# Kernel optimization log

Measured on AMD Instinct MI355X. Metric: run time of the kernel, lower is better.

## Reference

```python
import jax, jax.numpy as jnp
import numpy as np

B = 4096
D_FULL, D_T1, D_T2 = 1024, 512, 512
N_SPEC, N_SHARED = 4, 4
HID, OUT = 512, 256


def _expert_params(key, n_experts, d_in):
    k1, k2, k3, k4 = jax.random.split(key, 4)
    s1 = 1.0 / np.sqrt(d_in)
    s2 = 1.0 / np.sqrt(HID)
    return {
        'W1': jax.random.uniform(k1, (n_experts, d_in, HID), jnp.float32, -s1, s1),
        'b1': jax.random.uniform(k2, (n_experts, HID), jnp.float32, -s1, s1),
        'W2': jax.random.uniform(k3, (n_experts, HID, OUT), jnp.float32, -s2, s2),
        'b2': jax.random.uniform(k4, (n_experts, OUT), jnp.float32, -s2, s2),
    }


def setup_inputs() -> dict:
    key = jax.random.key(0)
    ks = jax.random.split(key, 12)
    x_full = jax.random.normal(ks[0], (B, D_FULL), jnp.float32)
    x_task1 = jax.random.normal(ks[1], (B, D_T1), jnp.float32)
    x_task2 = jax.random.normal(ks[2], (B, D_T2), jnp.float32)
    ps = _expert_params(ks[3], N_SHARED, D_FULL)
    p1 = _expert_params(ks[4], N_SPEC, D_T1)
    p2 = _expert_params(ks[5], N_SPEC, D_T2)
    sg = 1.0 / np.sqrt(D_FULL)
    s1 = 1.0 / np.sqrt(D_T1)
    s2 = 1.0 / np.sqrt(D_T2)
    return {
        'x_full': x_full, 'x_task1': x_task1, 'x_task2': x_task2,
        'sh_W1': ps['W1'], 'sh_b1': ps['b1'], 'sh_W2': ps['W2'], 'sh_b2': ps['b2'],
        't1_W1': p1['W1'], 't1_b1': p1['b1'], 't1_W2': p1['W2'], 't1_b2': p1['b2'],
        't2_W1': p2['W1'], 't2_b1': p2['b1'], 't2_W2': p2['W2'], 't2_b2': p2['b2'],
        'gsh_W': jax.random.uniform(ks[6], (D_FULL, 2 * N_SPEC + N_SHARED), jnp.float32, -sg, sg),
        'gsh_b': jax.random.uniform(ks[7], (2 * N_SPEC + N_SHARED,), jnp.float32, -sg, sg),
        'g1_W': jax.random.uniform(ks[8], (D_T1, N_SPEC + N_SHARED), jnp.float32, -s1, s1),
        'g1_b': jax.random.uniform(ks[9], (N_SPEC + N_SHARED,), jnp.float32, -s1, s1),
        'g2_W': jax.random.uniform(ks[10], (D_T2, N_SPEC + N_SHARED), jnp.float32, -s2, s2),
        'g2_b': jax.random.uniform(ks[11], (N_SPEC + N_SHARED,), jnp.float32, -s2, s2),
    }


def _experts(x, W1, b1, W2, b2):
    # x: [B, D]; W1: [E, D, H] -> out [E, B, OUT]
    h = jax.nn.relu(jnp.einsum('bd,edh->ebh', x, W1) + b1[:, None, :])
    return jax.nn.relu(jnp.einsum('ebh,eho->ebo', h, W2) + b2[:, None, :])


def reference(x_full, x_task1, x_task2,
              sh_W1, sh_b1, sh_W2, sh_b2,
              t1_W1, t1_b1, t1_W2, t1_b2,
              t2_W1, t2_b1, t2_W2, t2_b2,
              gsh_W, gsh_b, g1_W, g1_b, g2_W, g2_b):
    eo_shared = _experts(x_full, sh_W1, sh_b1, sh_W2, sh_b2)    # [Es, B, OUT]
    eo_t1 = _experts(x_task1, t1_W1, t1_b1, t1_W2, t1_b2)       # [Et, B, OUT]
    eo_t2 = _experts(x_task2, t2_W1, t2_b1, t2_W2, t2_b2)       # [Et, B, OUT]

    g1 = jax.nn.softmax(x_task1 @ g1_W + g1_b, axis=1)          # [B, Et+Es]
    out1 = jnp.einsum('ebc,be->bc', jnp.concatenate([eo_t1, eo_shared], axis=0), g1)

    g2 = jax.nn.softmax(x_task2 @ g2_W + g2_b, axis=1)
    out2 = jnp.einsum('ebc,be->bc', jnp.concatenate([eo_t2, eo_shared], axis=0), g2)

    gsh = jax.nn.softmax(x_full @ gsh_W + gsh_b, axis=1)        # [B, 2Et+Es]
    out_sh = jnp.einsum('ebc,be->bc', jnp.concatenate([eo_t1, eo_t2, eo_shared], axis=0), gsh)

    return (out_sh, out1, out2)
```

## Files before the change

### kernel.cpp

```cpp
#include <hip/hip_runtime.h>

typedef unsigned short u16;
typedef __attribute__((ext_vector_type(8))) short short8;
typedef __attribute__((ext_vector_type(4))) float f32x4;

#define GL2LDS16(src, dst) __builtin_amdgcn_global_load_lds( \
    (const __attribute__((address_space(1))) void*)(src),    \
    (__attribute__((address_space(3))) void*)(dst), 16, 0, 0)

__device__ __forceinline__ u16 f2bf(float f) {
  union { float f; unsigned u; } v; v.f = f;
  unsigned r = v.u + 0x7fffu + ((v.u >> 16) & 1u);
  return (u16)(r >> 16);
}
__device__ __forceinline__ float bf2f(u16 h) {
  union { unsigned u; float f; } v; v.u = ((unsigned)h) << 16; return v.f;
}

__global__ void k_gates_cvt(const float* __restrict__ xf, const float* __restrict__ x1,
                            const float* __restrict__ x2,
                            const float* __restrict__ gshW, const float* __restrict__ gshB,
                            const float* __restrict__ g1W, const float* __restrict__ g1B,
                            const float* __restrict__ g2W, const float* __restrict__ g2B,
                            u16* __restrict__ xfb, u16* __restrict__ x1b, u16* __restrict__ x2b,
                            float* __restrict__ gsh, float* __restrict__ g1o,
                            float* __restrict__ g2o) {
  const int b = blockIdx.x, lane = threadIdx.x;
  float s[12];
#pragma unroll
  for (int j = 0; j < 12; ++j) s[j] = 0.f;
  {
    const float* xr = xf + (size_t)b * 1024;
    u16* xw = xfb + (size_t)b * 1024;
    for (int k = lane; k < 1024; k += 64) {
      float v = xr[k];
      xw[k] = f2bf(v);
      const float* wr = gshW + (size_t)k * 12;
#pragma unroll
      for (int j = 0; j < 12; ++j) s[j] += v * wr[j];
    }
  }
  float u[8], w[8];
#pragma unroll
  for (int j = 0; j < 8; ++j) { u[j] = 0.f; w[j] = 0.f; }
  {
    const float* xr1 = x1 + (size_t)b * 512;
    const float* xr2 = x2 + (size_t)b * 512;
    u16* xw1 = x1b + (size_t)b * 512;
    u16* xw2 = x2b + (size_t)b * 512;
    for (int k = lane; k < 512; k += 64) {
      float v1 = xr1[k], v2 = xr2[k];
      xw1[k] = f2bf(v1); xw2[k] = f2bf(v2);
      const float* w1r = g1W + (size_t)k * 8;
      const float* w2r = g2W + (size_t)k * 8;
#pragma unroll
      for (int j = 0; j < 8; ++j) { u[j] += v1 * w1r[j]; w[j] += v2 * w2r[j]; }
    }
  }
#pragma unroll
  for (int off = 32; off >= 1; off >>= 1) {
#pragma unroll
    for (int j = 0; j < 12; ++j) s[j] += __shfl_xor(s[j], off, 64);
#pragma unroll
    for (int j = 0; j < 8; ++j) { u[j] += __shfl_xor(u[j], off, 64); w[j] += __shfl_xor(w[j], off, 64); }
  }
  if (lane == 0) {
    float m = -1e30f, tot = 0.f;
#pragma unroll
    for (int j = 0; j < 12; ++j) { s[j] += gshB[j]; m = fmaxf(m, s[j]); }
#pragma unroll
    for (int j = 0; j < 12; ++j) { s[j] = __expf(s[j] - m); tot += s[j]; }
    float inv = 1.f / tot;
#pragma unroll
    for (int j = 0; j < 12; ++j) gsh[(size_t)b * 12 + j] = s[j] * inv;
    m = -1e30f; tot = 0.f;
#pragma unroll
    for (int j = 0; j < 8; ++j) { u[j] += g1B[j]; m = fmaxf(m, u[j]); }
#pragma unroll
    for (int j = 0; j < 8; ++j) { u[j] = __expf(u[j] - m); tot += u[j]; }
    inv = 1.f / tot;
#pragma unroll
    for (int j = 0; j < 8; ++j) g1o[(size_t)b * 8 + j] = u[j] * inv;
    m = -1e30f; tot = 0.f;
#pragma unroll
    for (int j = 0; j < 8; ++j) { w[j] += g2B[j]; m = fmaxf(m, w[j]); }
#pragma unroll
    for (int j = 0; j < 8; ++j) { w[j] = __expf(w[j] - m); tot += w[j]; }
    inv = 1.f / tot;
#pragma unroll
    for (int j = 0; j < 8; ++j) g2o[(size_t)b * 8 + j] = w[j] * inv;
  }
}

struct TD { const float* src; u16* dst; int lgTps; int lgNtx; int R; int C; int tileBase; };
struct TArgs { TD d[6]; };

__global__ void k_transpose_all(TArgs ta) {
  __shared__ float tile[32][33];
  const int x = blockIdx.x;
  int di = 0;
#pragma unroll
  for (int i = 1; i < 6; ++i)
    if (x >= ta.d[i].tileBase) di = i;
  TD d = ta.d[di];
  const int local = x - d.tileBase;
  const int slice = local >> d.lgTps;
  const int ti = local & ((1 << d.lgTps) - 1);
  const int tx = ti & ((1 << d.lgNtx) - 1);
  const int ty = ti >> d.lgNtx;
  const float* src = d.src + (size_t)slice * d.R * d.C;
  u16* dst = d.dst + (size_t)slice * d.R * d.C;
  const int c0 = tx * 32, r0 = ty * 32;
  const int ttx = threadIdx.x, tty = threadIdx.y;
#pragma unroll
  for (int i = tty; i < 32; i += 8)
    tile[i][ttx] = src[(size_t)(r0 + i) * d.C + (c0 + ttx)];
  __syncthreads();
#pragma unroll
  for (int i = tty; i < 32; i += 8)
    dst[(size_t)(c0 + i) * d.R + (r0 + ttx)] = f2bf(tile[ttx][i]);
}

struct GemmDesc {
  const u16* A;
  const u16* BT;
  const float* bias;
  u16* C;
  int K;
  int N;
};
struct GemmArgs { GemmDesc d[12]; };

__global__ __launch_bounds__(512) void k_gemm8(GemmArgs args) {
  __shared__ __align__(16) u16 As[3 * 16384];
  __shared__ __align__(16) u16 Bs[3 * 8192];

  GemmDesc g = args.d[blockIdx.y];
  const int K = g.K, N = g.N;
  const int ntN = N >> 7;
  const int lg = (ntN == 4) ? 2 : 1;
  const int bx = blockIdx.x;
  const int row0 = (bx >> lg) << 8;
  const int col0 = (bx & (ntN - 1)) << 7;

  const int tid = threadIdx.x;
  const int lane = tid & 63;
  const int wid = tid >> 6;
  const int wm = wid >> 1;
  const int wn = wid & 1;
  const int lrow = lane & 15;
  const int lkq = lane >> 4;
  const int sw = lrow & 7;
  const int cx0 = lkq ^ sw;
  const int cx1 = (4 | lkq) ^ sw;

  int aoffs[4], boffs[4];
#pragma unroll
  for (int m = 0; m < 4; ++m) aoffs[m] = ((wm << 6) + (m << 4) + lrow) << 3;
#pragma unroll
  for (int n = 0; n < 4; ++n) boffs[n] = ((wn << 6) + (n << 4) + lrow) << 3;

  auto stageA = [&](int s, int kt, int j) {
    const int cb = (j << 9) + (wid << 6);
    const int c = cb + lane;
    const int r = c >> 3;
    const int gch = (c & 7) ^ (r & 7);
    GL2LDS16(g.A + (size_t)(row0 + r) * K + (kt << 6) + (gch << 3),
             &As[s * 16384 + cb * 8]);
  };
  auto stageB = [&](int s, int kt, int j) {
    const int cb = (j << 9) + (wid << 6);
    const int c = cb + lane;
    const int r = c >> 3;
    const int gch = (c & 7) ^ (r & 7);
    GL2LDS16(g.BT + (size_t)(col0 + r) * K + (kt << 6) + (gch << 3),
             &Bs[s * 8192 + cb * 8]);
  };

  f32x4 acc[4][4];
#pragma unroll
  for (int m = 0; m < 4; ++m)
#pragma unroll
    for (int n = 0; n < 4; ++n)
      acc[m][n] = (f32x4){0.f, 0.f, 0.f, 0.f};

  const int T = K >> 6;
#pragma unroll
  for (int j = 0; j < 4; ++j) stageA(0, 0, j);
#pragma unroll
  for (int j = 0; j < 2; ++j) stageB(0, 0, j);
#pragma unroll
  for (int j = 0; j < 4; ++j) stageA(1, 1, j);
#pragma unroll
  for (int j = 0; j < 2; ++j) stageB(1, 1, j);
  asm volatile("s_waitcnt vmcnt(6)" ::: "memory");
  __builtin_amdgcn_s_barrier();

  int slot = 0;
  for (int t = 0; t < T; ++t) {
    const u16* Asl = &As[slot * 16384];
    const u16* Bsl = &Bs[slot * 8192];
    const int s2 = (slot >= 1) ? slot - 1 : 2;
    short8 a[4], b[4];

#pragma unroll
    for (int m = 0; m < 4; ++m) a[m] = *(const short8*)&Asl[(aoffs[m] | cx0) << 3];
#pragma unroll
    for (int n = 0; n < 4; ++n) b[n] = *(const short8*)&Bsl[(boffs[n] | cx0) << 3];
    if (t + 2 < T) { stageA(s2, t + 2, 0); stageA(s2, t + 2, 1); stageB(s2, t + 2, 0); }
    __builtin_amdgcn_s_barrier();
    asm volatile("s_waitcnt lgkmcnt(0)" ::: "memory");
    __builtin_amdgcn_sched_barrier(0);
    __builtin_amdgcn_s_setprio(1);
#pragma unroll
    for (int m = 0; m < 4; ++m)
#pragma unroll
      for (int n = 0; n < 4; ++n)
        acc[m][n] = __builtin_amdgcn_mfma_f32_16x16x32_bf16(a[m], b[n], acc[m][n], 0, 0, 0);
    __builtin_amdgcn_s_setprio(0);
    __builtin_amdgcn_s_barrier();

#pragma unroll
    for (int m = 0; m < 4; ++m) a[m] = *(const short8*)&Asl[(aoffs[m] | cx1) << 3];
#pragma unroll
    for (int n = 0; n < 4; ++n) b[n] = *(const short8*)&Bsl[(boffs[n] | cx1) << 3];
    if (t + 2 < T) { stageA(s2, t + 2, 2); stageA(s2, t + 2, 3); stageB(s2, t + 2, 1); }
    __builtin_amdgcn_s_barrier();
    asm volatile("s_waitcnt lgkmcnt(0)" ::: "memory");
    __builtin_amdgcn_sched_barrier(0);
    __builtin_amdgcn_s_setprio(1);
#pragma unroll
    for (int m = 0; m < 4; ++m)
#pragma unroll
      for (int n = 0; n < 4; ++n)
        acc[m][n] = __builtin_amdgcn_mfma_f32_16x16x32_bf16(a[m], b[n], acc[m][n], 0, 0, 0);
    __builtin_amdgcn_s_setprio(0);
    asm volatile("s_waitcnt vmcnt(6)" ::: "memory");
    __builtin_amdgcn_s_barrier();

    slot = (slot == 2) ? 0 : slot + 1;
  }

  const int rb = lkq << 2;
#pragma unroll
  for (int n = 0; n < 4; ++n) {
    const int gc = col0 + (wn << 6) + (n << 4) + lrow;
    const float bv = g.bias[gc];
#pragma unroll
    for (int m = 0; m < 4; ++m) {
      const int gr = row0 + (wm << 6) + (m << 4) + rb;
#pragma unroll
      for (int j = 0; j < 4; ++j) {
        float o = fmaxf(acc[m][n][j] + bv, 0.f);
        g.C[(size_t)(gr + j) * N + gc] = f2bf(o);
      }
    }
  }
}

__global__ void k_reduce(const u16* __restrict__ OutB, const float* __restrict__ gsh,
                         const float* __restrict__ g1, const float* __restrict__ g2,
                         float* __restrict__ out) {
  int t = blockIdx.x * 256 + threadIdx.x;
  int b = t >> 5;
  int c0 = (t & 31) << 3;
  float wsh[12], w1[8], w2[8];
#pragma unroll
  for (int j = 0; j < 12; ++j) wsh[j] = gsh[(size_t)b * 12 + j];
#pragma unroll
  for (int j = 0; j < 8; ++j) { w1[j] = g1[(size_t)b * 8 + j]; w2[j] = g2[(size_t)b * 8 + j]; }
  float ash[8] = {0, 0, 0, 0, 0, 0, 0, 0};
  float a1[8] = {0, 0, 0, 0, 0, 0, 0, 0};
  float a2[8] = {0, 0, 0, 0, 0, 0, 0, 0};
#pragma unroll
  for (int e = 0; e < 12; ++e) {
    short8 v = *(const short8*)&OutB[((size_t)e * 4096 + b) * 256 + c0];
    float f[8];
#pragma unroll
    for (int i = 0; i < 8; ++i) f[i] = bf2f((u16)v[i]);
#pragma unroll
    for (int i = 0; i < 8; ++i) ash[i] += wsh[e] * f[i];
    if (e < 4) {
#pragma unroll
      for (int i = 0; i < 8; ++i) a1[i] += w1[e] * f[i];
    } else if (e < 8) {
#pragma unroll
      for (int i = 0; i < 8; ++i) a2[i] += w2[e - 4] * f[i];
    } else {
#pragma unroll
      for (int i = 0; i < 8; ++i) a1[i] += w1[e - 4] * f[i];
#pragma unroll
      for (int i = 0; i < 8; ++i) a2[i] += w2[e - 4] * f[i];
    }
  }
  size_t base = (size_t)b * 256 + c0;
  float4* o;
  o = (float4*)(out + base);
  o[0] = make_float4(ash[0], ash[1], ash[2], ash[3]);
  o[1] = make_float4(ash[4], ash[5], ash[6], ash[7]);
  o = (float4*)(out + 4096ull * 256 + base);
  o[0] = make_float4(a1[0], a1[1], a1[2], a1[3]);
  o[1] = make_float4(a1[4], a1[5], a1[6], a1[7]);
  o = (float4*)(out + 2ull * 4096 * 256 + base);
  o[0] = make_float4(a2[0], a2[1], a2[2], a2[3]);
  o[1] = make_float4(a2[4], a2[5], a2[6], a2[7]);
}

extern "C" void kernel_launch(void* const* d_in, const int* in_sizes, int n_in,
                              void* d_out, int out_size, void* d_ws, size_t ws_size,
                              hipStream_t stream) {
  const float* x_full = (const float*)d_in[0];
  const float* x_t1 = (const float*)d_in[1];
  const float* x_t2 = (const float*)d_in[2];
  const float* sh_W1 = (const float*)d_in[3];
  const float* sh_b1 = (const float*)d_in[4];
  const float* sh_W2 = (const float*)d_in[5];
  const float* sh_b2 = (const float*)d_in[6];
  const float* t1_W1 = (const float*)d_in[7];
  const float* t1_b1 = (const float*)d_in[8];
  const float* t1_W2 = (const float*)d_in[9];
  const float* t1_b2 = (const float*)d_in[10];
  const float* t2_W1 = (const float*)d_in[11];
  const float* t2_b1 = (const float*)d_in[12];
  const float* t2_W2 = (const float*)d_in[13];
  const float* t2_b2 = (const float*)d_in[14];
  const float* gsh_W = (const float*)d_in[15];
  const float* gsh_b = (const float*)d_in[16];
  const float* g1_W = (const float*)d_in[17];
  const float* g1_b = (const float*)d_in[18];
  const float* g2_W = (const float*)d_in[19];
  const float* g2_b = (const float*)d_in[20];

  char* ws = (char*)d_ws;
  size_t off = 0;
  auto alloc = [&](size_t bytes) -> void* {
    void* p = ws + off;
    off += (bytes + 255) & ~(size_t)255;
    return p;
  };
  u16* xf_b = (u16*)alloc(4096ull * 1024 * 2);
  u16* x1_b = (u16*)alloc(4096ull * 512 * 2);
  u16* x2_b = (u16*)alloc(4096ull * 512 * 2);
  u16* w1t_t1 = (u16*)alloc(4ull * 512 * 512 * 2);
  u16* w1t_t2 = (u16*)alloc(4ull * 512 * 512 * 2);
  u16* w1t_sh = (u16*)alloc(4ull * 512 * 1024 * 2);
  u16* w2t = (u16*)alloc(12ull * 256 * 512 * 2);
  u16* H = (u16*)alloc(12ull * 4096 * 512 * 2);
  u16* OutB = (u16*)alloc(12ull * 4096 * 256 * 2);
  float* gshv = (float*)alloc(4096ull * 12 * 4);
  float* g1v = (float*)alloc(4096ull * 8 * 4);
  float* g2v = (float*)alloc(4096ull * 8 * 4);

  k_gates_cvt<<<4096, 64, 0, stream>>>(x_full, x_t1, x_t2, gsh_W, gsh_b, g1_W, g1_b, g2_W, g2_b,
                                       xf_b, x1_b, x2_b, gshv, g1v, g2v);

  TArgs ta;
  ta.d[0] = TD{t1_W1, w1t_t1, 8, 4, 512, 512, 0};
  ta.d[1] = TD{t2_W1, w1t_t2, 8, 4, 512, 512, 1024};
  ta.d[2] = TD{sh_W1, w1t_sh, 9, 4, 1024, 512, 2048};
  ta.d[3] = TD{t1_W2, w2t, 7, 3, 512, 256, 4096};
  ta.d[4] = TD{t2_W2, w2t + 4ull * 256 * 512, 7, 3, 512, 256, 4608};
  ta.d[5] = TD{sh_W2, w2t + 8ull * 256 * 512, 7, 3, 512, 256, 5120};
  k_transpose_all<<<5632, dim3(32, 8), 0, stream>>>(ta);

  GemmArgs ga1;
  for (int e = 0; e < 4; ++e) {
    ga1.d[e] = GemmDesc{xf_b, w1t_sh + (size_t)e * 512 * 1024, sh_b1 + e * 512,
                        H + (size_t)(8 + e) * 4096 * 512, 1024, 512};
    ga1.d[4 + e] = GemmDesc{x1_b, w1t_t1 + (size_t)e * 512 * 512, t1_b1 + e * 512,
                            H + (size_t)e * 4096 * 512, 512, 512};
    ga1.d[8 + e] = GemmDesc{x2_b, w1t_t2 + (size_t)e * 512 * 512, t2_b1 + e * 512,
                            H + (size_t)(4 + e) * 4096 * 512, 512, 512};
  }
  k_gemm8<<<dim3(64, 12), 512, 0, stream>>>(ga1);

  GemmArgs ga2;
  for (int e = 0; e < 12; ++e) {
    const float* bias = (e < 4) ? (t1_b2 + e * 256)
                      : (e < 8) ? (t2_b2 + (e - 4) * 256)
                                : (sh_b2 + (e - 8) * 256);
    ga2.d[e] = GemmDesc{H + (size_t)e * 4096 * 512, w2t + (size_t)e * 256 * 512, bias,
                        OutB + (size_t)e * 4096 * 256, 512, 256};
  }
  k_gemm8<<<dim3(32, 12), 512, 0, stream>>>(ga2);

  k_reduce<<<512, 256, 0, stream>>>(OutB, gshv, g1v, g2v, (float*)d_out);
}
```

Baseline: 117.9 us.

## Replace 256x128 GEMM tile with 256x256 tile and double-buffered half-stage pipeline

The batched expert GEMM kernel now uses 256x256 output tiles per 512-thread block (8x4 MFMA accumulators per wave) instead of 256x128. The LDS staging becomes two buffers, with A and B loaded in halves interleaved across eight phases per two K-steps, and uses new swizzle patterns. The larger tile raises arithmetic intensity and halves the number of blocks. In exchange, register pressure is higher, only one block fits per CU, and grids shrink to 384 and 192 blocks, which may underfill the 256 CUs.

```diff
diff --git a/kernel.cpp b/kernel.cpp
--- a/kernel.cpp
+++ b/kernel.cpp
@@ -128,130 +128,131 @@
   u16* C;
   int K;
   int N;
+  int iters;
 };
 struct GemmArgs { GemmDesc d[12]; };
 
-__global__ __launch_bounds__(512) void k_gemm8(GemmArgs args) {
-  __shared__ __align__(16) u16 As[3 * 16384];
-  __shared__ __align__(16) u16 Bs[3 * 8192];
+#define PHASE(BUF, KS, MH, ...)                                                   \
+  {                                                                               \
+    const char* AsB = (const char*)As + (BUF) * 32768;                            \
+    const char* BsB = (const char*)Bs + (BUF) * 32768 + (KS) * 16384;             \
+    if ((MH) == 0) {                                                              \
+      _Pragma("unroll") for (int ni = 0; ni < 4; ++ni)                            \
+          b[ni] = *(const short8*)(BsB + boff[ni]);                               \
+    }                                                                             \
+    _Pragma("unroll") for (int q = 0; q < 4; ++q)                                 \
+        a[q] = *(const short8*)(AsB + (aoff[(MH) * 4 + q] ^ ((KS) * 64)));        \
+    __VA_ARGS__;                                                                  \
+    __builtin_amdgcn_s_barrier();                                                 \
+    asm volatile("s_waitcnt lgkmcnt(0)" ::: "memory");                            \
+    __builtin_amdgcn_sched_barrier(0);                                            \
+    __builtin_amdgcn_s_setprio(1);                                                \
+    _Pragma("unroll") for (int q = 0; q < 4; ++q)                                 \
+        _Pragma("unroll") for (int ni = 0; ni < 4; ++ni)                          \
+            acc[(MH) * 4 + q][ni] = __builtin_amdgcn_mfma_f32_16x16x32_bf16(      \
+                a[q], b[ni], acc[(MH) * 4 + q][ni], 0, 0, 0);                     \
+    __builtin_amdgcn_s_setprio(0);                                                \
+  }
+
+__global__ __launch_bounds__(512, 1) void k_gemm256(GemmArgs args) {
+  __shared__ __align__(16) u16 As[32768];
+  __shared__ __align__(16) u16 Bs[32768];
 
   GemmDesc g = args.d[blockIdx.y];
-  const int K = g.K, N = g.N;
-  const int ntN = N >> 7;
-  const int lg = (ntN == 4) ? 2 : 1;
+  const int K = g.K, N = g.N, iters = g.iters;
+  const int ntN = N >> 8;
+  const int lg = (ntN == 2) ? 1 : 0;
   const int bx = blockIdx.x;
   const int row0 = (bx >> lg) << 8;
-  const int col0 = (bx & (ntN - 1)) << 7;
+  const int col0 = (bx & (ntN - 1)) << 8;
 
   const int tid = threadIdx.x;
   const int lane = tid & 63;
   const int wid = tid >> 6;
-  const int wm = wid >> 1;
-  const int wn = wid & 1;
+  const int wm = wid & 1;
+  const int wn = wid >> 1;
   const int lrow = lane & 15;
   const int lkq = lane >> 4;
-  const int sw = lrow & 7;
-  const int cx0 = lkq ^ sw;
-  const int cx1 = (4 | lkq) ^ sw;
-
-  int aoffs[4], boffs[4];
-#pragma unroll
-  for (int m = 0; m < 4; ++m) aoffs[m] = ((wm << 6) + (m << 4) + lrow) << 3;
-#pragma unroll
-  for (int n = 0; n < 4; ++n) boffs[n] = ((wn << 6) + (n << 4) + lrow) << 3;
-
-  auto stageA = [&](int s, int kt, int j) {
-    const int cb = (j << 9) + (wid << 6);
-    const int c = cb + lane;
-    const int r = c >> 3;
-    const int gch = (c & 7) ^ (r & 7);
-    GL2LDS16(g.A + (size_t)(row0 + r) * K + (kt << 6) + (gch << 3),
-             &As[s * 16384 + cb * 8]);
+
+  int aoff[8], boff[4];
+#pragma unroll
+  for (int mi = 0; mi < 8; ++mi)
+    aoff[mi] = wm * 16384 + (mi * 16 + lrow) * 128 + ((lkq ^ (lrow & 7)) * 16);
+#pragma unroll
+  for (int ni = 0; ni < 4; ++ni)
+    boff[ni] = (wn * 64 + ni * 16 + lrow) * 64 + ((lkq ^ ((lrow >> 1) & 3)) * 16);
+
+  auto stageAhalf = [&](int buf, int half, int kt) {
+#pragma unroll
+    for (int j = 0; j < 2; ++j) {
+      const int cb = (wid * 2 + j) * 64;
+      const int c = cb + lane;
+      const int r = c >> 3;
+      const int cir = (c & 7) ^ (r & 7);
+      GL2LDS16(g.A + (size_t)(row0 + half * 128 + r) * K + kt * 64 + cir * 8,
+               &As[(buf * 2048 + half * 1024 + cb) * 8]);
+    }
   };
-  auto stageB = [&](int s, int kt, int j) {
-    const int cb = (j << 9) + (wid << 6);
-    const int c = cb + lane;
-    const int r = c >> 3;
-    const int gch = (c & 7) ^ (r & 7);
-    GL2LDS16(g.BT + (size_t)(col0 + r) * K + (kt << 6) + (gch << 3),
-             &Bs[s * 8192 + cb * 8]);
+  auto stageBhalf = [&](int buf, int ks, int kt) {
+#pragma unroll
+    for (int j = 0; j < 2; ++j) {
+      const int cb = (wid * 2 + j) * 64;
+      const int c = cb + lane;
+      const int r = c >> 2;
+      const int cir = (c & 3) ^ ((r >> 1) & 3);
+      GL2LDS16(g.BT + (size_t)(col0 + r) * K + kt * 64 + ks * 32 + cir * 8,
+               &Bs[(buf * 2048 + ks * 1024 + cb) * 8]);
+    }
   };
 
-  f32x4 acc[4][4];
-#pragma unroll
-  for (int m = 0; m < 4; ++m)
+  f32x4 acc[8][4];
+#pragma unroll
+  for (int m = 0; m < 8; ++m)
 #pragma unroll
     for (int n = 0; n < 4; ++n)
       acc[m][n] = (f32x4){0.f, 0.f, 0.f, 0.f};
 
-  const int T = K >> 6;
-#pragma unroll
-  for (int j = 0; j < 4; ++j) stageA(0, 0, j);
-#pragma unroll
-  for (int j = 0; j < 2; ++j) stageB(0, 0, j);
-#pragma unroll
-  for (int j = 0; j < 4; ++j) stageA(1, 1, j);
-#pragma unroll
-  for (int j = 0; j < 2; ++j) stageB(1, 1, j);
-  asm volatile("s_waitcnt vmcnt(6)" ::: "memory");
+  stageBhalf(0, 0, 0); stageBhalf(0, 1, 0);
+  stageAhalf(0, 0, 0); stageAhalf(0, 1, 0);
+  stageBhalf(1, 0, 1); stageBhalf(1, 1, 1);
+  asm volatile("s_waitcnt vmcnt(4)" ::: "memory");
   __builtin_amdgcn_s_barrier();
 
-  int slot = 0;
-  for (int t = 0; t < T; ++t) {
-    const u16* Asl = &As[slot * 16384];
-    const u16* Bsl = &Bs[slot * 8192];
-    const int s2 = (slot >= 1) ? slot - 1 : 2;
-    short8 a[4], b[4];
-
-#pragma unroll
-    for (int m = 0; m < 4; ++m) a[m] = *(const short8*)&Asl[(aoffs[m] | cx0) << 3];
-#pragma unroll
-    for (int n = 0; n < 4; ++n) b[n] = *(const short8*)&Bsl[(boffs[n] | cx0) << 3];
-    if (t + 2 < T) { stageA(s2, t + 2, 0); stageA(s2, t + 2, 1); stageB(s2, t + 2, 0); }
-    __builtin_amdgcn_s_barrier();
-    asm volatile("s_waitcnt lgkmcnt(0)" ::: "memory");
-    __builtin_amdgcn_sched_barrier(0);
-    __builtin_amdgcn_s_setprio(1);
-#pragma unroll
-    for (int m = 0; m < 4; ++m)
-#pragma unroll
-      for (int n = 0; n < 4; ++n)
-        acc[m][n] = __builtin_amdgcn_mfma_f32_16x16x32_bf16(a[m], b[n], acc[m][n], 0, 0, 0);
-    __builtin_amdgcn_s_setprio(0);
-    __builtin_amdgcn_s_barrier();
-
-#pragma unroll
-    for (int m = 0; m < 4; ++m) a[m] = *(const short8*)&Asl[(aoffs[m] | cx1) << 3];
-#pragma unroll
-    for (int n = 0; n < 4; ++n) b[n] = *(const short8*)&Bsl[(boffs[n] | cx1) << 3];
-    if (t + 2 < T) { stageA(s2, t + 2, 2); stageA(s2, t + 2, 3); stageB(s2, t + 2, 1); }
-    __builtin_amdgcn_s_barrier();
-    asm volatile("s_waitcnt lgkmcnt(0)" ::: "memory");
-    __builtin_amdgcn_sched_barrier(0);
-    __builtin_amdgcn_s_setprio(1);
-#pragma unroll
-    for (int m = 0; m < 4; ++m)
-#pragma unroll
-      for (int n = 0; n < 4; ++n)
-        acc[m][n] = __builtin_amdgcn_mfma_f32_16x16x32_bf16(a[m], b[n], acc[m][n], 0, 0, 0);
-    __builtin_amdgcn_s_setprio(0);
-    asm volatile("s_waitcnt vmcnt(6)" ::: "memory");
-    __builtin_amdgcn_s_barrier();
-
-    slot = (slot == 2) ? 0 : slot + 1;
-  }
-
-  const int rb = lkq << 2;
-#pragma unroll
-  for (int n = 0; n < 4; ++n) {
-    const int gc = col0 + (wn << 6) + (n << 4) + lrow;
+  short8 a[4], b[4];
+  for (int i = 0; i < iters; ++i) {
+    const int t1 = 2 * i + 1;
+    const bool nl = (i + 1 < iters);
+    PHASE(0, 0, 0, stageAhalf(1, 0, t1));
+    __builtin_amdgcn_s_barrier();
+    PHASE(0, 0, 1, stageAhalf(1, 1, t1));
+    __builtin_amdgcn_s_barrier();
+    PHASE(0, 1, 0, if (nl) stageBhalf(0, 0, t1 + 1));
+    __builtin_amdgcn_s_barrier();
+    PHASE(0, 1, 1, if (nl) stageBhalf(0, 1, t1 + 1));
+    if (nl) { asm volatile("s_waitcnt vmcnt(4)" ::: "memory"); }
+    else    { asm volatile("s_waitcnt vmcnt(0)" ::: "memory"); }
+    __builtin_amdgcn_s_barrier();
+    PHASE(1, 0, 0, if (nl) stageAhalf(0, 0, t1 + 1));
+    __builtin_amdgcn_s_barrier();
+    PHASE(1, 0, 1, if (nl) stageAhalf(0, 1, t1 + 1));
+    __builtin_amdgcn_s_barrier();
+    PHASE(1, 1, 0, if (nl) stageBhalf(1, 0, t1 + 2));
+    __builtin_amdgcn_s_barrier();
+    PHASE(1, 1, 1, if (nl) stageBhalf(1, 1, t1 + 2));
+    asm volatile("s_waitcnt vmcnt(4)" ::: "memory");
+    __builtin_amdgcn_s_barrier();
+  }
+
+#pragma unroll
+  for (int ni = 0; ni < 4; ++ni) {
+    const int gc = col0 + wn * 64 + ni * 16 + lrow;
     const float bv = g.bias[gc];
 #pragma unroll
-    for (int m = 0; m < 4; ++m) {
-      const int gr = row0 + (wm << 6) + (m << 4) + rb;
+    for (int mi = 0; mi < 8; ++mi) {
+      const int gr = row0 + wm * 128 + mi * 16 + lkq * 4;
 #pragma unroll
       for (int j = 0; j < 4; ++j) {
-        float o = fmaxf(acc[m][n][j] + bv, 0.f);
+        float o = fmaxf(acc[mi][ni][j] + bv, 0.f);
         g.C[(size_t)(gr + j) * N + gc] = f2bf(o);
       }
     }
@@ -366,13 +367,13 @@
   GemmArgs ga1;
   for (int e = 0; e < 4; ++e) {
     ga1.d[e] = GemmDesc{xf_b, w1t_sh + (size_t)e * 512 * 1024, sh_b1 + e * 512,
-                        H + (size_t)(8 + e) * 4096 * 512, 1024, 512};
+                        H + (size_t)(8 + e) * 4096 * 512, 1024, 512, 8};
     ga1.d[4 + e] = GemmDesc{x1_b, w1t_t1 + (size_t)e * 512 * 512, t1_b1 + e * 512,
-                            H + (size_t)e * 4096 * 512, 512, 512};
+                            H + (size_t)e * 4096 * 512, 512, 512, 4};
     ga1.d[8 + e] = GemmDesc{x2_b, w1t_t2 + (size_t)e * 512 * 512, t2_b1 + e * 512,
-                            H + (size_t)(4 + e) * 4096 * 512, 512, 512};
-  }
-  k_gemm8<<<dim3(64, 12), 512, 0, stream>>>(ga1);
+                            H + (size_t)(4 + e) * 4096 * 512, 512, 512, 4};
+  }
+  k_gemm256<<<dim3(32, 12), 512, 0, stream>>>(ga1);
 
   GemmArgs ga2;
   for (int e = 0; e < 12; ++e) {
@@ -380,9 +381,9 @@
                       : (e < 8) ? (t2_b2 + (e - 4) * 256)
                                 : (sh_b2 + (e - 8) * 256);
     ga2.d[e] = GemmDesc{H + (size_t)e * 4096 * 512, w2t + (size_t)e * 256 * 512, bias,
-                        OutB + (size_t)e * 4096 * 256, 512, 256};
-  }
-  k_gemm8<<<dim3(32, 12), 512, 0, stream>>>(ga2);
+                        OutB + (size_t)e * 4096 * 256, 512, 256, 4};
+  }
+  k_gemm256<<<dim3(16, 12), 512, 0, stream>>>(ga2);
 
   k_reduce<<<512, 256, 0, stream>>>(OutB, gshv, g1v, g2v, (float*)d_out);
 }
```

Result: faster. 113.2 us (-4.0%).

## Replace 256x128 triple-buffered GEMM with 128x256 double-buffered BK=32 kernel

Applied to the files above, without the earlier changes.

The GEMM kernel moves from a 256x128 output tile with K-step 64 and a three-slot LDS pipeline to a 128x256 tile with K-step 32 and two buffers. LDS drops to 48KB per block, and launch_bounds(512,4) asks for higher occupancy. Each iteration now ends with a full vmcnt(0) wait and a barrier, and the loop trip count T is passed in from the host. The aim is more resident blocks to hide latency, at the cost of more barriers per unit of K and a shallower prefetch.

```diff
diff --git a/kernel.cpp b/kernel.cpp
--- a/kernel.cpp
+++ b/kernel.cpp
@@ -128,53 +128,60 @@
   u16* C;
   int K;
   int N;
+  int T;
 };
 struct GemmArgs { GemmDesc d[12]; };
 
-__global__ __launch_bounds__(512) void k_gemm8(GemmArgs args) {
-  __shared__ __align__(16) u16 As[3 * 16384];
-  __shared__ __align__(16) u16 Bs[3 * 8192];
+#define BARR __builtin_amdgcn_s_barrier()
+#define WAITL0                                                   \
+  {                                                              \
+    asm volatile("s_waitcnt lgkmcnt(0)" ::: "memory");           \
+    __builtin_amdgcn_sched_barrier(0);                           \
+  }
+#define WAITV0 asm volatile("s_waitcnt vmcnt(0)" ::: "memory")
+
+__global__ __launch_bounds__(512, 4) void k_gemm128(GemmArgs args) {
+  __shared__ __align__(16) u16 As[2 * 128 * 32];
+  __shared__ __align__(16) u16 Bs[2 * 256 * 32];
 
   GemmDesc g = args.d[blockIdx.y];
-  const int K = g.K, N = g.N;
-  const int ntN = N >> 7;
-  const int lg = (ntN == 4) ? 2 : 1;
+  const int K = g.K, N = g.N, T = g.T;
+  const int ntN = N >> 8;
   const int bx = blockIdx.x;
-  const int row0 = (bx >> lg) << 8;
-  const int col0 = (bx & (ntN - 1)) << 7;
+  const int nt = bx & (ntN - 1);
+  const int bt = (ntN == 2) ? (bx >> 1) : bx;
+  const int row0 = bt << 7;
+  const int col0 = nt << 8;
 
   const int tid = threadIdx.x;
   const int lane = tid & 63;
   const int wid = tid >> 6;
-  const int wm = wid >> 1;
-  const int wn = wid & 1;
+  const int wm = wid & 1;
+  const int wn = wid >> 1;
   const int lrow = lane & 15;
   const int lkq = lane >> 4;
-  const int sw = lrow & 7;
-  const int cx0 = lkq ^ sw;
-  const int cx1 = (4 | lkq) ^ sw;
-
-  int aoffs[4], boffs[4];
-#pragma unroll
-  for (int m = 0; m < 4; ++m) aoffs[m] = ((wm << 6) + (m << 4) + lrow) << 3;
-#pragma unroll
-  for (int n = 0; n < 4; ++n) boffs[n] = ((wn << 6) + (n << 4) + lrow) << 3;
-
-  auto stageA = [&](int s, int kt, int j) {
-    const int cb = (j << 9) + (wid << 6);
-    const int c = cb + lane;
-    const int r = c >> 3;
-    const int gch = (c & 7) ^ (r & 7);
-    GL2LDS16(g.A + (size_t)(row0 + r) * K + (kt << 6) + (gch << 3),
-             &As[s * 16384 + cb * 8]);
-  };
-  auto stageB = [&](int s, int kt, int j) {
-    const int cb = (j << 9) + (wid << 6);
-    const int c = cb + lane;
-    const int r = c >> 3;
-    const int gch = (c & 7) ^ (r & 7);
-    GL2LDS16(g.BT + (size_t)(col0 + r) * K + (kt << 6) + (gch << 3),
-             &Bs[s * 8192 + cb * 8]);
+
+  const int csw = (lkq ^ (lrow & 3)) * 16;
+  int aoff[4], boff[4];
+#pragma unroll
+  for (int mi = 0; mi < 4; ++mi) aoff[mi] = (wm * 64 + mi * 16 + lrow) * 64 + csw;
+#pragma unroll
+  for (int ni = 0; ni < 4; ++ni) boff[ni] = (wn * 64 + ni * 16 + lrow) * 64 + csw;
+
+  const int ar = tid >> 2;
+  const int acs = (tid & 3) ^ (ar & 3);
+  const u16* aSrc = g.A + (size_t)(row0 + ar) * K + acs * 8;
+  const int br0 = tid >> 2;
+  const int bc0 = (tid & 3) ^ (br0 & 3);
+  const u16* bSrc0 = g.BT + (size_t)(col0 + br0) * K + bc0 * 8;
+  const int br1 = 128 + (tid >> 2);
+  const int bc1 = (tid & 3) ^ (br1 & 3);
+  const u16* bSrc1 = g.BT + (size_t)(col0 + br1) * K + bc1 * 8;
+
+  auto STAGE = [&](int buf, int t) {
+    GL2LDS16(aSrc + (size_t)t * 32, &As[buf * 4096 + tid * 8]);
+    GL2LDS16(bSrc0 + (size_t)t * 32, &Bs[buf * 8192 + tid * 8]);
+    GL2LDS16(bSrc1 + (size_t)t * 32, &Bs[buf * 8192 + 4096 + tid * 8]);
   };
 
   f32x4 acc[4][4];
@@ -184,74 +191,52 @@
     for (int n = 0; n < 4; ++n)
       acc[m][n] = (f32x4){0.f, 0.f, 0.f, 0.f};
 
-  const int T = K >> 6;
-#pragma unroll
-  for (int j = 0; j < 4; ++j) stageA(0, 0, j);
-#pragma unroll
-  for (int j = 0; j < 2; ++j) stageB(0, 0, j);
-#pragma unroll
-  for (int j = 0; j < 4; ++j) stageA(1, 1, j);
-#pragma unroll
-  for (int j = 0; j < 2; ++j) stageB(1, 1, j);
-  asm volatile("s_waitcnt vmcnt(6)" ::: "memory");
-  __builtin_amdgcn_s_barrier();
-
-  int slot = 0;
+  STAGE(0, 0);
+  WAITV0;
+  BARR;
+
   for (int t = 0; t < T; ++t) {
-    const u16* Asl = &As[slot * 16384];
-    const u16* Bsl = &Bs[slot * 8192];
-    const int s2 = (slot >= 1) ? slot - 1 : 2;
-    short8 a[4], b[4];
-
-#pragma unroll
-    for (int m = 0; m < 4; ++m) a[m] = *(const short8*)&Asl[(aoffs[m] | cx0) << 3];
-#pragma unroll
-    for (int n = 0; n < 4; ++n) b[n] = *(const short8*)&Bsl[(boffs[n] | cx0) << 3];
-    if (t + 2 < T) { stageA(s2, t + 2, 0); stageA(s2, t + 2, 1); stageB(s2, t + 2, 0); }
-    __builtin_amdgcn_s_barrier();
-    asm volatile("s_waitcnt lgkmcnt(0)" ::: "memory");
-    __builtin_amdgcn_sched_barrier(0);
+    const int buf = t & 1;
+    const char* Ab = (const char*)As + buf * 8192;
+    const char* Bb = (const char*)Bs + buf * 16384;
+    short8 a0, a1, b[4];
+#pragma unroll
+    for (int ni = 0; ni < 4; ++ni) b[ni] = *(const short8*)(Bb + boff[ni]);
+    a0 = *(const short8*)(Ab + aoff[0]);
+    a1 = *(const short8*)(Ab + aoff[1]);
+    if (t + 1 < T) STAGE(buf ^ 1, t + 1);
+    WAITL0;
     __builtin_amdgcn_s_setprio(1);
 #pragma unroll
-    for (int m = 0; m < 4; ++m)
-#pragma unroll
-      for (int n = 0; n < 4; ++n)
-        acc[m][n] = __builtin_amdgcn_mfma_f32_16x16x32_bf16(a[m], b[n], acc[m][n], 0, 0, 0);
+    for (int ni = 0; ni < 4; ++ni) {
+      acc[0][ni] = __builtin_amdgcn_mfma_f32_16x16x32_bf16(a0, b[ni], acc[0][ni], 0, 0, 0);
+      acc[1][ni] = __builtin_amdgcn_mfma_f32_16x16x32_bf16(a1, b[ni], acc[1][ni], 0, 0, 0);
+    }
     __builtin_amdgcn_s_setprio(0);
-    __builtin_amdgcn_s_barrier();
-
-#pragma unroll
-    for (int m = 0; m < 4; ++m) a[m] = *(const short8*)&Asl[(aoffs[m] | cx1) << 3];
-#pragma unroll
-    for (int n = 0; n < 4; ++n) b[n] = *(const short8*)&Bsl[(boffs[n] | cx1) << 3];
-    if (t + 2 < T) { stageA(s2, t + 2, 2); stageA(s2, t + 2, 3); stageB(s2, t + 2, 1); }
-    __builtin_amdgcn_s_barrier();
-    asm volatile("s_waitcnt lgkmcnt(0)" ::: "memory");
-    __builtin_amdgcn_sched_barrier(0);
+    a0 = *(const short8*)(Ab + aoff[2]);
+    a1 = *(const short8*)(Ab + aoff[3]);
+    WAITL0;
     __builtin_amdgcn_s_setprio(1);
 #pragma unroll
-    for (int m = 0; m < 4; ++m)
-#pragma unroll
-      for (int n = 0; n < 4; ++n)
-        acc[m][n] = __builtin_amdgcn_mfma_f32_16x16x32_bf16(a[m], b[n], acc[m][n], 0, 0, 0);
+    for (int ni = 0; ni < 4; ++ni) {
+      acc[2][ni] = __builtin_amdgcn_mfma_f32_16x16x32_bf16(a0, b[ni], acc[2][ni], 0, 0, 0);
+      acc[3][ni] = __builtin_amdgcn_mfma_f32_16x16x32_bf16(a1, b[ni], acc[3][ni], 0, 0, 0);
+    }
     __builtin_amdgcn_s_setprio(0);
-    asm volatile("s_waitcnt vmcnt(6)" ::: "memory");
-    __builtin_amdgcn_s_barrier();
-
-    slot = (slot == 2) ? 0 : slot + 1;
-  }
-
-  const int rb = lkq << 2;
-#pragma unroll
-  for (int n = 0; n < 4; ++n) {
-    const int gc = col0 + (wn << 6) + (n << 4) + lrow;
+    WAITV0;
+    BARR;
+  }
+
+#pragma unroll
+  for (int ni = 0; ni < 4; ++ni) {
+    const int gc = col0 + wn * 64 + ni * 16 + lrow;
     const float bv = g.bias[gc];
 #pragma unroll
-    for (int m = 0; m < 4; ++m) {
-      const int gr = row0 + (wm << 6) + (m << 4) + rb;
+    for (int mi = 0; mi < 4; ++mi) {
+      const int gr = row0 + wm * 64 + mi * 16 + lkq * 4;
 #pragma unroll
       for (int j = 0; j < 4; ++j) {
-        float o = fmaxf(acc[m][n][j] + bv, 0.f);
+        float o = fmaxf(acc[mi][ni][j] + bv, 0.f);
         g.C[(size_t)(gr + j) * N + gc] = f2bf(o);
       }
     }
@@ -366,13 +351,13 @@
   GemmArgs ga1;
   for (int e = 0; e < 4; ++e) {
     ga1.d[e] = GemmDesc{xf_b, w1t_sh + (size_t)e * 512 * 1024, sh_b1 + e * 512,
-                        H + (size_t)(8 + e) * 4096 * 512, 1024, 512};
+                        H + (size_t)(8 + e) * 4096 * 512, 1024, 512, 32};
     ga1.d[4 + e] = GemmDesc{x1_b, w1t_t1 + (size_t)e * 512 * 512, t1_b1 + e * 512,
-                            H + (size_t)e * 4096 * 512, 512, 512};
+                            H + (size_t)e * 4096 * 512, 512, 512, 16};
     ga1.d[8 + e] = GemmDesc{x2_b, w1t_t2 + (size_t)e * 512 * 512, t2_b1 + e * 512,
-                            H + (size_t)(4 + e) * 4096 * 512, 512, 512};
-  }
-  k_gemm8<<<dim3(64, 12), 512, 0, stream>>>(ga1);
+                            H + (size_t)(4 + e) * 4096 * 512, 512, 512, 16};
+  }
+  k_gemm128<<<dim3(64, 12), 512, 0, stream>>>(ga1);
 
   GemmArgs ga2;
   for (int e = 0; e < 12; ++e) {
@@ -380,9 +365,9 @@
                       : (e < 8) ? (t2_b2 + (e - 4) * 256)
                                 : (sh_b2 + (e - 8) * 256);
     ga2.d[e] = GemmDesc{H + (size_t)e * 4096 * 512, w2t + (size_t)e * 256 * 512, bias,
-                        OutB + (size_t)e * 4096 * 256, 512, 256};
-  }
-  k_gemm8<<<dim3(32, 12), 512, 0, stream>>>(ga2);
+                        OutB + (size_t)e * 4096 * 256, 512, 256, 16};
+  }
+  k_gemm128<<<dim3(32, 12), 512, 0, stream>>>(ga2);
 
   k_reduce<<<512, 256, 0, stream>>>(OutB, gshv, g1v, g2v, (float*)d_out);
 }
```

Result: faster. 108.0 us (-8.4%).
